# Kernel optimization log

Measured on AMD Instinct MI355X. Metric: run time of the kernel, lower is better.

The kernel has to match this reference:

```python
import jax, jax.numpy as jnp
import numpy as np

K, N = 4096, 4096
GROUP_SIZE = 128
N_GROUPS = N // GROUP_SIZE  # 32
B, S = 4, 2048
NBITS = 4


def setup_inputs() -> dict:
    key = jax.random.key(0)
    ks = jax.random.split(key, 7)
    x = jax.random.normal(ks[0], (B, S, N), dtype=jnp.float32)
    W_q = jax.random.randint(ks[1], (K, N), 0, 2 ** NBITS, dtype=jnp.int32)
    # positive per-group scales, zeros in quant range
    scales = jax.random.uniform(ks[2], (K, N_GROUPS, 1), dtype=jnp.float32, minval=0.005, maxval=0.05)
    zeros = jax.random.uniform(ks[3], (K, N_GROUPS, 1), dtype=jnp.float32, minval=0.0, maxval=float(2 ** NBITS - 1))
    mu1 = jax.random.uniform(ks[4], (N,), dtype=jnp.float32, minval=0.5, maxval=1.5)
    mu2 = jax.random.uniform(ks[5], (K,), dtype=jnp.float32, minval=0.5, maxval=1.5)
    bias = jax.random.normal(ks[6], (K,), dtype=jnp.float32)
    return {"x": x, "W_q": W_q, "scales": scales, "zeros": zeros, "mu1": mu1, "mu2": mu2, "bias": bias}


def reference(x, W_q, scales, zeros, mu1, mu2, bias):
    input_dtype = x.dtype
    n_groups = scales.shape[1]
    group_size = W_q.shape[1] // n_groups
    # group-wise dequant: (Q - zero) * scale
    Q_g = W_q.astype(jnp.float32).reshape(K, n_groups, group_size)
    W_deq_norm = (Q_g - zeros) * scales  # [K, n_groups, group_size]
    # mu1/mu2 rescale (inverse Sinkhorn normalization)
    W_deq = W_deq_norm.reshape(K, N) * mu2[:, None] * mu1[None, :]
    W_deq = W_deq.astype(input_dtype)
    # F.linear(x, W, b) = x @ W.T + b -> out [B, S, K]
    return jnp.einsum('bsn,kn->bsk', x, W_deq) + bias.astype(input_dtype)
```

## Files before the change

### kernel.cpp

```cpp
#include <hip/hip_runtime.h>
#include <hip/hip_bf16.h>
#include <stdint.h>

#define M_ROWS 8192
#define K_OUT  4096
#define N_RED  4096
#define NGRP   32

#define BM 256
#define BN 256
#define BK 64
#define NKT (N_RED / BK)

typedef __attribute__((ext_vector_type(8))) __bf16 bf16x8;
typedef __attribute__((ext_vector_type(4))) float   f32x4;


__device__ __forceinline__ unsigned short f32_to_bf16_rn(float f) {
  uint32_t u = __float_as_uint(f);
  uint32_t r = (u + 0x7FFFu + ((u >> 16) & 1u)) >> 16;
  return (unsigned short)r;
}

__device__ __forceinline__ void async_copy16(const void* gsrc, void* lds_base) {
  __builtin_amdgcn_global_load_lds(
      (const __attribute__((address_space(1))) uint32_t*)gsrc,
      (__attribute__((address_space(3))) uint32_t*)lds_base,
      16 , 0, 0);
}

constexpr size_t XCHUNKS = (size_t)M_ROWS * N_RED / 8;
constexpr size_t WCHUNKS = (size_t)K_OUT * N_RED / 8;

__global__ __launch_bounds__(256) void prep_kernel(
    const float* __restrict__ x, const int* __restrict__ Wq,
    const float* __restrict__ scales, const float* __restrict__ zeros,
    const float* __restrict__ mu1, const float* __restrict__ mu2,
    unsigned short* __restrict__ xb, unsigned short* __restrict__ Wb) {
  const size_t stride = (size_t)gridDim.x * 256;
  for (size_t c = (size_t)blockIdx.x * 256 + threadIdx.x;
       c < XCHUNKS + WCHUNKS; c += stride) {
    if (c < XCHUNKS) {
      const float4* xp = (const float4*)(x + c * 8);
      float4 v0 = xp[0];
      float4 v1 = xp[1];
      union { unsigned short h[8]; uint4 v; } p;
      p.h[0] = f32_to_bf16_rn(v0.x); p.h[1] = f32_to_bf16_rn(v0.y);
      p.h[2] = f32_to_bf16_rn(v0.z); p.h[3] = f32_to_bf16_rn(v0.w);
      p.h[4] = f32_to_bf16_rn(v1.x); p.h[5] = f32_to_bf16_rn(v1.y);
      p.h[6] = f32_to_bf16_rn(v1.z); p.h[7] = f32_to_bf16_rn(v1.w);
      *(uint4*)(xb + c * 8) = p.v;
    } else {
      size_t idx = c - XCHUNKS;
      int k = (int)(idx >> 9);
      int n = (int)(idx & 511) << 3;
      int g = n >> 7;
      float s  = scales[k * NGRP + g];
      float z  = zeros[k * NGRP + g];
      float sm = s * mu2[k];
      const int4* qp = (const int4*)(Wq + (size_t)k * N_RED + n);
      int4 q0 = qp[0];
      int4 q1 = qp[1];
      const float4* mp = (const float4*)(mu1 + n);
      float4 m0 = mp[0];
      float4 m1 = mp[1];
      union { unsigned short h[8]; uint4 v; } p;
      p.h[0] = f32_to_bf16_rn(((float)q0.x - z) * sm * m0.x);
      p.h[1] = f32_to_bf16_rn(((float)q0.y - z) * sm * m0.y);
      p.h[2] = f32_to_bf16_rn(((float)q0.z - z) * sm * m0.z);
      p.h[3] = f32_to_bf16_rn(((float)q0.w - z) * sm * m0.w);
      p.h[4] = f32_to_bf16_rn(((float)q1.x - z) * sm * m1.x);
      p.h[5] = f32_to_bf16_rn(((float)q1.y - z) * sm * m1.y);
      p.h[6] = f32_to_bf16_rn(((float)q1.z - z) * sm * m1.z);
      p.h[7] = f32_to_bf16_rn(((float)q1.w - z) * sm * m1.w);
      *(uint4*)(Wb + (size_t)k * N_RED + n) = p.v;
    }
  }
}

__global__ __launch_bounds__(512, 2) void gemm8_kernel(
    const unsigned short* __restrict__ A, const unsigned short* __restrict__ B,
    const float* __restrict__ bias, float* __restrict__ C) {
  __shared__ __align__(16) unsigned short lds[2][32768];

  const int bid = blockIdx.x;
  const int wg = (bid & 7) * 64 + (bid >> 3);
  const int tileM = wg >> 4;
  const int tileN = wg & 15;

  const int tid  = threadIdx.x;
  const int wave = tid >> 6;
  const int lane = tid & 63;
  const int wm = wave >> 2;
  const int wn = wave & 3;
  const int fr = lane & 15;
  const int fq = lane >> 4;

  const unsigned short* Ag = A + (size_t)(tileM * BM) * N_RED;
  const unsigned short* Bg = B + (size_t)(tileN * BN) * N_RED;

  const unsigned short* srcA[2];
  const unsigned short* srcB[2];
#pragma unroll
  for (int l = 0; l < 2; ++l) {
    int f = l * 512 + tid;
    int row = (f >> 6) * 16 + (f & 15);
    int kc8 = ((f >> 4) & 3) * 8;
    srcA[l] = Ag + (size_t)row * N_RED + kc8;
    srcB[l] = Bg + (size_t)row * N_RED + kc8;
  }

  f32x4 acc[8][4] = {};
  bf16x8 af[8], bfr[2];

#define STAGE_A(nb, kk)                                                       \
  do {                                                                        \
    async_copy16(srcA[0] + (kk) * 32, &lds[nb][(kk) * 8192 + wave * 512]);    \
    async_copy16(srcA[1] + (kk) * 32,                                         \
                 &lds[nb][(kk) * 8192 + 4096 + wave * 512]);                  \
  } while (0)
#define STAGE_B(nb, kk)                                                       \
  do {                                                                        \
    async_copy16(srcB[0] + (kk) * 32,                                         \
                 &lds[nb][16384 + (kk) * 8192 + wave * 512]);                 \
    async_copy16(srcB[1] + (kk) * 32,                                         \
                 &lds[nb][16384 + (kk) * 8192 + 4096 + wave * 512]);          \
  } while (0)

#define READ_A(cb, kk)                                                        \
  do {                                                                        \
    _Pragma("unroll") for (int m = 0; m < 8; ++m) af[m] =                     \
        *(const bf16x8*)&lds[cb][(kk) * 8192 + (wm * 8 + m) * 512 + lane * 8];\
  } while (0)

#define READ_B(cb, kk, nh)                                                    \
  do {                                                                        \
    bfr[0] = *(const bf16x8*)&lds[cb][16384 + (kk) * 8192 +                   \
                                      (wn * 4 + (nh) * 2) * 512 + lane * 8];  \
    bfr[1] = *(const bf16x8*)&lds[cb][16384 + (kk) * 8192 +                   \
                                      (wn * 4 + (nh) * 2 + 1) * 512 +         \
                                      lane * 8];                              \
  } while (0)

#define MFMA_BLK(nh)                                                          \
  do {                                                                        \
    __builtin_amdgcn_s_setprio(1);                                            \
    _Pragma("unroll") for (int m = 0; m < 8; ++m) {                           \
      acc[m][(nh) * 2] = __builtin_amdgcn_mfma_f32_16x16x32_bf16(             \
          af[m], bfr[0], acc[m][(nh) * 2], 0, 0, 0);                          \
      acc[m][(nh) * 2 + 1] = __builtin_amdgcn_mfma_f32_16x16x32_bf16(         \
          af[m], bfr[1], acc[m][(nh) * 2 + 1], 0, 0, 0);                      \
    }                                                                         \
    __builtin_amdgcn_s_setprio(0);                                            \
  } while (0)

  STAGE_A(0, 0);
  STAGE_B(0, 0);
  STAGE_A(0, 1);
  STAGE_B(0, 1);
  srcA[0] += BK; srcA[1] += BK; srcB[0] += BK; srcB[1] += BK;

  for (int t = 0; t < NKT - 1; ++t) {
    const int cb = t & 1, nb = cb ^ 1;
    asm volatile("s_waitcnt vmcnt(4)" ::: "memory");
    __builtin_amdgcn_s_barrier();
    __builtin_amdgcn_sched_barrier(0);
    READ_A(cb, 0);
    READ_B(cb, 0, 0);
    STAGE_A(nb, 0);
    MFMA_BLK(0);
    __builtin_amdgcn_s_barrier();
    __builtin_amdgcn_sched_barrier(0);
    READ_B(cb, 0, 1);
    STAGE_B(nb, 0);
    MFMA_BLK(1);
    asm volatile("s_waitcnt vmcnt(4)" ::: "memory");
    __builtin_amdgcn_s_barrier();
    __builtin_amdgcn_sched_barrier(0);
    READ_A(cb, 1);
    READ_B(cb, 1, 0);
    STAGE_A(nb, 1);
    MFMA_BLK(0);
    __builtin_amdgcn_s_barrier();
    __builtin_amdgcn_sched_barrier(0);
    READ_B(cb, 1, 1);
    STAGE_B(nb, 1);
    MFMA_BLK(1);
    srcA[0] += BK; srcA[1] += BK; srcB[0] += BK; srcB[1] += BK;
  }
  {
    const int cb = (NKT - 1) & 1;
    asm volatile("s_waitcnt vmcnt(4)" ::: "memory");
    __builtin_amdgcn_s_barrier();
    __builtin_amdgcn_sched_barrier(0);
    READ_A(cb, 0); READ_B(cb, 0, 0); MFMA_BLK(0);
    __builtin_amdgcn_s_barrier();
    __builtin_amdgcn_sched_barrier(0);
    READ_B(cb, 0, 1); MFMA_BLK(1);
    asm volatile("s_waitcnt vmcnt(0)" ::: "memory");
    __builtin_amdgcn_s_barrier();
    __builtin_amdgcn_sched_barrier(0);
    READ_A(cb, 1); READ_B(cb, 1, 0); MFMA_BLK(0);
    __builtin_amdgcn_s_barrier();
    __builtin_amdgcn_sched_barrier(0);
    READ_B(cb, 1, 1); MFMA_BLK(1);
  }

  float bv[4];
#pragma unroll
  for (int n = 0; n < 4; ++n)
    bv[n] = bias[tileN * BN + wn * 64 + n * 16 + fr];
#pragma unroll
  for (int m = 0; m < 8; ++m) {
    int row0 = tileM * BM + wm * 128 + m * 16 + fq * 4;
#pragma unroll
    for (int j = 0; j < 4; ++j) {
      float* crow = C + (size_t)(row0 + j) * K_OUT + tileN * BN + wn * 64 + fr;
#pragma unroll
      for (int n = 0; n < 4; ++n)
        crow[n * 16] = acc[m][n][j] + bv[n];
    }
  }
#undef STAGE_A
#undef STAGE_B
#undef READ_A
#undef READ_B
#undef MFMA_BLK
}

extern "C" void kernel_launch(void* const* d_in, const int* in_sizes, int n_in,
                              void* d_out, int out_size, void* d_ws, size_t ws_size,
                              hipStream_t stream) {
  const float* x      = (const float*)d_in[0];
  const int*   Wq     = (const int*)d_in[1];
  const float* scales = (const float*)d_in[2];
  const float* zeros  = (const float*)d_in[3];
  const float* mu1    = (const float*)d_in[4];
  const float* mu2    = (const float*)d_in[5];
  const float* bias   = (const float*)d_in[6];
  float* out = (float*)d_out;

  unsigned short* xb = (unsigned short*)d_ws;
  unsigned short* Wb = (unsigned short*)((char*)d_ws +
                         (size_t)M_ROWS * N_RED * sizeof(unsigned short));

  prep_kernel<<<2048, 256, 0, stream>>>(x, Wq, scales, zeros, mu1, mu2, xb, Wb);
  gemm8_kernel<<<(M_ROWS / BM) * (K_OUT / BN), 512, 0, stream>>>(xb, Wb, bias, out);
}
```

Before: 545.1 us.

## Swizzle LDS tile layout and restructure MFMA pipeline into 4x4 blocks

Changes the LDS staging layout to a row-major 64-byte-per-row tile with an XOR swizzle, so each lane reads its fragment from a permuted address and bank conflicts drop. The inner loop now loads 4 A and 4 B fragments and issues a 4x4 MFMA block per half, instead of 8 A by 2 B, and the schedule adds explicit lgkmcnt waits and extra barriers. This lowers fragment register pressure and LDS conflicts, at the cost of more barriers per K-step.

```diff
diff --git a/kernel.cpp b/kernel.cpp
--- a/kernel.cpp
+++ b/kernel.cpp
@@ -81,7 +81,7 @@
 __global__ __launch_bounds__(512, 2) void gemm8_kernel(
     const unsigned short* __restrict__ A, const unsigned short* __restrict__ B,
     const float* __restrict__ bias, float* __restrict__ C) {
-  __shared__ __align__(16) unsigned short lds[2][32768];
+  __shared__ __align__(16) unsigned short lds[2][4][8192];
 
   const int bid = blockIdx.x;
   const int wg = (bid & 7) * 64 + (bid >> 3);
@@ -96,114 +96,113 @@
   const int fr = lane & 15;
   const int fq = lane >> 4;
 
-  const unsigned short* Ag = A + (size_t)(tileM * BM) * N_RED;
-  const unsigned short* Bg = B + (size_t)(tileN * BN) * N_RED;
+  const int laneoff =
+      (fr * 64 + fq * 16) ^ ((fr & 8) << 2) ^ ((fr & 4) << 2);
 
   const unsigned short* srcA[2];
   const unsigned short* srcB[2];
 #pragma unroll
   for (int l = 0; l < 2; ++l) {
-    int f = l * 512 + tid;
-    int row = (f >> 6) * 16 + (f & 15);
-    int kc8 = ((f >> 4) & 3) * 8;
-    srcA[l] = Ag + (size_t)row * N_RED + kc8;
-    srcB[l] = Bg + (size_t)row * N_RED + kc8;
-  }
+    int a = (l * 512 + tid) * 16;
+    int q = a ^ (((a >> 9) & 1) << 5) ^ (((a >> 8) & 1) << 4);
+    int row = q >> 6;
+    int ce  = (q & 63) >> 1;
+    srcA[l] = A + (size_t)(tileM * BM + row) * N_RED + ce;
+    srcB[l] = B + (size_t)(tileN * BN + row) * N_RED + ce;
+  }
+  const int dst0 = wave * 512;
+  const int dst1 = 4096 + wave * 512;
 
   f32x4 acc[8][4] = {};
-  bf16x8 af[8], bfr[2];
+  bf16x8 af[4], bfr[4];
 
 #define STAGE_A(nb, kk)                                                       \
   do {                                                                        \
-    async_copy16(srcA[0] + (kk) * 32, &lds[nb][(kk) * 8192 + wave * 512]);    \
-    async_copy16(srcA[1] + (kk) * 32,                                         \
-                 &lds[nb][(kk) * 8192 + 4096 + wave * 512]);                  \
+    async_copy16(srcA[0] + (kk) * 32, &lds[nb][(kk) * 2][dst0]);              \
+    async_copy16(srcA[1] + (kk) * 32, &lds[nb][(kk) * 2][dst1]);              \
   } while (0)
 #define STAGE_B(nb, kk)                                                       \
   do {                                                                        \
-    async_copy16(srcB[0] + (kk) * 32,                                         \
-                 &lds[nb][16384 + (kk) * 8192 + wave * 512]);                 \
-    async_copy16(srcB[1] + (kk) * 32,                                         \
-                 &lds[nb][16384 + (kk) * 8192 + 4096 + wave * 512]);          \
-  } while (0)
-
-#define READ_A(cb, kk)                                                        \
-  do {                                                                        \
-    _Pragma("unroll") for (int m = 0; m < 8; ++m) af[m] =                     \
-        *(const bf16x8*)&lds[cb][(kk) * 8192 + (wm * 8 + m) * 512 + lane * 8];\
-  } while (0)
-
-#define READ_B(cb, kk, nh)                                                    \
-  do {                                                                        \
-    bfr[0] = *(const bf16x8*)&lds[cb][16384 + (kk) * 8192 +                   \
-                                      (wn * 4 + (nh) * 2) * 512 + lane * 8];  \
-    bfr[1] = *(const bf16x8*)&lds[cb][16384 + (kk) * 8192 +                   \
-                                      (wn * 4 + (nh) * 2 + 1) * 512 +         \
-                                      lane * 8];                              \
-  } while (0)
-
-#define MFMA_BLK(nh)                                                          \
+    async_copy16(srcB[0] + (kk) * 32, &lds[nb][(kk) * 2 + 1][dst0]);          \
+    async_copy16(srcB[1] + (kk) * 32, &lds[nb][(kk) * 2 + 1][dst1]);          \
+  } while (0)
+
+#define READ_A4(cb, kk, mh)                                                   \
+  do {                                                                        \
+    const char* ab = (const char*)&lds[cb][(kk) * 2][0] + wm * 8192 +         \
+                     (mh) * 4096 + laneoff;                                   \
+    _Pragma("unroll") for (int m = 0; m < 4; ++m)                             \
+        af[m] = *(const bf16x8*)(ab + m * 1024);                              \
+  } while (0)
+#define READ_B4(cb, kk)                                                       \
+  do {                                                                        \
+    const char* bb_ = (const char*)&lds[cb][(kk) * 2 + 1][0] + wn * 4096 +    \
+                      laneoff;                                                \
+    _Pragma("unroll") for (int n = 0; n < 4; ++n)                             \
+        bfr[n] = *(const bf16x8*)(bb_ + n * 1024);                            \
+  } while (0)
+
+#define MFMA16(mh)                                                            \
   do {                                                                        \
     __builtin_amdgcn_s_setprio(1);                                            \
-    _Pragma("unroll") for (int m = 0; m < 8; ++m) {                           \
-      acc[m][(nh) * 2] = __builtin_amdgcn_mfma_f32_16x16x32_bf16(             \
-          af[m], bfr[0], acc[m][(nh) * 2], 0, 0, 0);                          \
-      acc[m][(nh) * 2 + 1] = __builtin_amdgcn_mfma_f32_16x16x32_bf16(         \
-          af[m], bfr[1], acc[m][(nh) * 2 + 1], 0, 0, 0);                      \
-    }                                                                         \
+    _Pragma("unroll") for (int m = 0; m < 4; ++m)                             \
+        _Pragma("unroll") for (int n = 0; n < 4; ++n)                         \
+            acc[(mh) * 4 + m][n] = __builtin_amdgcn_mfma_f32_16x16x32_bf16(   \
+                af[m], bfr[n], acc[(mh) * 4 + m][n], 0, 0, 0);                \
     __builtin_amdgcn_s_setprio(0);                                            \
   } while (0)
+
+#define BAR()   __builtin_amdgcn_s_barrier()
+#define SBAR()  __builtin_amdgcn_sched_barrier(0)
+#define LGKM0() asm volatile("s_waitcnt lgkmcnt(0)" ::: "memory")
+#define VM(n)   asm volatile("s_waitcnt vmcnt(" #n ")" ::: "memory")
 
   STAGE_A(0, 0);
   STAGE_B(0, 0);
   STAGE_A(0, 1);
   STAGE_B(0, 1);
   srcA[0] += BK; srcA[1] += BK; srcB[0] += BK; srcB[1] += BK;
+  VM(4);
+  BAR();
+  SBAR();
 
   for (int t = 0; t < NKT - 1; ++t) {
     const int cb = t & 1, nb = cb ^ 1;
-    asm volatile("s_waitcnt vmcnt(4)" ::: "memory");
-    __builtin_amdgcn_s_barrier();
-    __builtin_amdgcn_sched_barrier(0);
-    READ_A(cb, 0);
-    READ_B(cb, 0, 0);
-    STAGE_A(nb, 0);
-    MFMA_BLK(0);
-    __builtin_amdgcn_s_barrier();
-    __builtin_amdgcn_sched_barrier(0);
-    READ_B(cb, 0, 1);
-    STAGE_B(nb, 0);
-    MFMA_BLK(1);
-    asm volatile("s_waitcnt vmcnt(4)" ::: "memory");
-    __builtin_amdgcn_s_barrier();
-    __builtin_amdgcn_sched_barrier(0);
-    READ_A(cb, 1);
-    READ_B(cb, 1, 0);
-    STAGE_A(nb, 1);
-    MFMA_BLK(0);
-    __builtin_amdgcn_s_barrier();
-    __builtin_amdgcn_sched_barrier(0);
-    READ_B(cb, 1, 1);
-    STAGE_B(nb, 1);
-    MFMA_BLK(1);
+    READ_A4(cb, 0, 0); READ_B4(cb, 0); STAGE_A(nb, 0);
+    BAR(); LGKM0(); SBAR();
+    MFMA16(0);
+    BAR(); SBAR();
+    READ_A4(cb, 0, 1); STAGE_B(nb, 0);
+    BAR(); LGKM0(); SBAR();
+    MFMA16(1);
+    VM(4); BAR(); SBAR();
+    READ_A4(cb, 1, 0); READ_B4(cb, 1); STAGE_A(nb, 1);
+    BAR(); LGKM0(); SBAR();
+    MFMA16(0);
+    BAR(); SBAR();
+    READ_A4(cb, 1, 1); STAGE_B(nb, 1);
+    BAR(); LGKM0(); SBAR();
+    MFMA16(1);
+    VM(4); BAR(); SBAR();
     srcA[0] += BK; srcA[1] += BK; srcB[0] += BK; srcB[1] += BK;
   }
   {
     const int cb = (NKT - 1) & 1;
-    asm volatile("s_waitcnt vmcnt(4)" ::: "memory");
-    __builtin_amdgcn_s_barrier();
-    __builtin_amdgcn_sched_barrier(0);
-    READ_A(cb, 0); READ_B(cb, 0, 0); MFMA_BLK(0);
-    __builtin_amdgcn_s_barrier();
-    __builtin_amdgcn_sched_barrier(0);
-    READ_B(cb, 0, 1); MFMA_BLK(1);
-    asm volatile("s_waitcnt vmcnt(0)" ::: "memory");
-    __builtin_amdgcn_s_barrier();
-    __builtin_amdgcn_sched_barrier(0);
-    READ_A(cb, 1); READ_B(cb, 1, 0); MFMA_BLK(0);
-    __builtin_amdgcn_s_barrier();
-    __builtin_amdgcn_sched_barrier(0);
-    READ_B(cb, 1, 1); MFMA_BLK(1);
+    READ_A4(cb, 0, 0); READ_B4(cb, 0);
+    BAR(); LGKM0(); SBAR();
+    MFMA16(0);
+    BAR(); SBAR();
+    READ_A4(cb, 0, 1);
+    BAR(); LGKM0(); SBAR();
+    MFMA16(1);
+    VM(0); BAR(); SBAR();
+    READ_A4(cb, 1, 0); READ_B4(cb, 1);
+    BAR(); LGKM0(); SBAR();
+    MFMA16(0);
+    BAR(); SBAR();
+    READ_A4(cb, 1, 1);
+    BAR(); LGKM0(); SBAR();
+    MFMA16(1);
   }
 
   float bv[4];
@@ -223,9 +222,13 @@
   }
 #undef STAGE_A
 #undef STAGE_B
-#undef READ_A
-#undef READ_B
-#undef MFMA_BLK
+#undef READ_A4
+#undef READ_B4
+#undef MFMA16
+#undef BAR
+#undef SBAR
+#undef LGKM0
+#undef VM
 }
 
 extern "C" void kernel_launch(void* const* d_in, const int* in_sizes, int n_in,
```

New measurement: 524.6 us. -3.8%, faster.
